# Performance work log

Hardware: AMD Instinct MI355X
Metric: run time of the kernel (lower is better)

## Reference

```python
import jax, jax.numpy as jnp
import numpy as np

B, H, W = 4, 1024, 1024

# 8-tap Sobel-style stencil: offsets in (u, v) units of (dx, dy)
OFF_U = jnp.array([-1.0, -1.0, -1.0, 0.0, 0.0, 1.0, 1.0, 1.0], dtype=jnp.float32)
OFF_V = jnp.array([-1.0, 0.0, 1.0, -1.0, 1.0, -1.0, 0.0, 1.0], dtype=jnp.float32)
KU = jnp.array([-0.25, -0.5, -0.25, 0.0, 0.0, 0.25, 0.5, 0.25], dtype=jnp.float32)
KV = jnp.array([-0.25, 0.0, 0.25, -0.5, 0.5, -0.25, 0.0, 0.25], dtype=jnp.float32)


def setup_inputs() -> dict:
    key = jax.random.key(0)
    k1, k2 = jax.random.split(key)
    x = jax.random.uniform(k1, (B, 3, H, W), dtype=jnp.float32)
    sigma = jax.random.uniform(k2, (B,), dtype=jnp.float32) * 2.0 + 0.5  # pixels
    return {"x": x, "sigma": sigma}


def _bilinear(tex, u, v):
    # tex: [3, H, W]; u, v: [8, H, W] normalized UV in [0,1]
    Hh, Ww = tex.shape[1], tex.shape[2]
    px = u * Ww - 0.5
    py = v * Hh - 0.5
    x0 = jnp.floor(px)
    y0 = jnp.floor(py)
    fx = (px - x0)[None]  # [1,8,H,W]
    fy = (py - y0)[None]
    x0i = jnp.clip(x0.astype(jnp.int32), 0, Ww - 1)
    x1i = jnp.clip(x0i + 1, 0, Ww - 1)
    y0i = jnp.clip(y0.astype(jnp.int32), 0, Hh - 1)
    y1i = jnp.clip(y0i + 1, 0, Hh - 1)
    t00 = tex[:, y0i, x0i]  # [3,8,H,W]
    t01 = tex[:, y0i, x1i]
    t10 = tex[:, y1i, x0i]
    t11 = tex[:, y1i, x1i]
    return (t00 * (1 - fx) * (1 - fy) + t01 * fx * (1 - fy)
            + t10 * (1 - fx) * fy + t11 * fx * fy)


def reference(x, sigma):
    Bb, C, Hh, Ww = x.shape
    ys, xs = jnp.meshgrid(jnp.arange(Hh, dtype=x.dtype),
                          jnp.arange(Ww, dtype=x.dtype), indexing='ij')
    u0 = (xs + 0.5) / Ww  # pixel-center UV
    v0 = (ys + 0.5) / Hh
    dx = sigma / Ww  # [B]
    dy = sigma / Hh
    u = u0[None, None] + OFF_U[None, :, None, None] * dx[:, None, None, None]  # [B,8,H,W]
    v = v0[None, None] + OFF_V[None, :, None, None] * dy[:, None, None, None]
    s = jax.vmap(_bilinear)(x, u, v)  # [B,3,8,H,W]
    s_u = jnp.einsum('bcthw,t->bchw', s, KU)
    s_v = jnp.einsum('bcthw,t->bchw', s, KV)
    lum = jnp.array([100.0, 1.0, 1.0], dtype=x.dtype)[None, :, None, None]
    s_u = s_u * lum
    s_v = s_v * lum
    # structure tensor components E, G, F
    return jnp.stack([(s_u * s_u).sum(1), (s_v * s_v).sum(1), (s_u * s_v).sum(1)], axis=1)
```

## Files before the change

kernel.cpp:

```cpp
#include <hip/hip_runtime.h>


#define W_ 1024
#define H_ 1024
#define PLANE (1 << 20)
#define TCOLS 64
#define TROWS 32
#define ROWS 8
#define LSTRIDE 72
#define NTILES 4
#define BUFSZ 9232

#define BX_ROWS 128
#define BX_SLOTS 134
#define BX_CH 1072
#define BX_NG 804

__device__ __forceinline__ float lerp1(float a, float b, float f) {
    return fmaf(f, b - a, a);
}

__device__ __forceinline__ void async_copy16(const float* g, float* s) {
    __builtin_amdgcn_global_load_lds(
        (const __attribute__((address_space(1))) unsigned int*)g,
        (__attribute__((address_space(3))) unsigned int*)s,
        16, 0, 0);
}

__device__ void slow_pixel(const float* __restrict__ Xb, float* __restrict__ Ob,
                           float sg, int xi, int y)
{
    float imf = floorf(-sg), ipf = floorf(sg);
    float fm  = -sg - imf;
    float fp  =  sg - ipf;
    int   im  = (int)imf, ip = (int)ipf;

    int cm0 = min(max(xi + im, 0), W_ - 1), cm1 = min(cm0 + 1, W_ - 1);
    int cp0 = min(max(xi + ip, 0), W_ - 1), cp1 = min(cp0 + 1, W_ - 1);
    int rm0 = min(max(y + im, 0), H_ - 1),  rm1 = min(rm0 + 1, H_ - 1);
    int rp0 = min(max(y + ip, 0), H_ - 1),  rp1 = min(rp0 + 1, H_ - 1);

    int o_rm0 = rm0 << 10, o_rm1 = rm1 << 10;
    int o_rp0 = rp0 << 10, o_rp1 = rp1 << 10;
    int o_r0  = y   << 10;

    float oxx = 0.f, oyy = 0.f, oxy = 0.f;

    #pragma unroll
    for (int c = 0; c < 3; ++c) {
        const float* base = Xb + ((size_t)c << 20);

        float hm_m0 = lerp1(base[o_rm0 + cm0], base[o_rm0 + cm1], fm);
        float hm_m1 = lerp1(base[o_rm1 + cm0], base[o_rm1 + cm1], fm);
        float hm_0  = lerp1(base[o_r0  + cm0], base[o_r0  + cm1], fm);
        float hm_p0 = lerp1(base[o_rp0 + cm0], base[o_rp0 + cm1], fm);
        float hm_p1 = lerp1(base[o_rp1 + cm0], base[o_rp1 + cm1], fm);
        float hp_m0 = lerp1(base[o_rm0 + cp0], base[o_rm0 + cp1], fp);
        float hp_m1 = lerp1(base[o_rm1 + cp0], base[o_rm1 + cp1], fp);
        float hp_0  = lerp1(base[o_r0  + cp0], base[o_r0  + cp1], fp);
        float hp_p0 = lerp1(base[o_rp0 + cp0], base[o_rp0 + cp1], fp);
        float hp_p1 = lerp1(base[o_rp1 + cp0], base[o_rp1 + cp1], fp);
        float h0_m0 = base[o_rm0 + xi], h0_m1 = base[o_rm1 + xi];
        float h0_p0 = base[o_rp0 + xi], h0_p1 = base[o_rp1 + xi];

        float t0 = lerp1(hm_m0, hm_m1, fm);
        float t1 = hm_0;
        float t2 = lerp1(hm_p0, hm_p1, fp);
        float t3 = lerp1(h0_m0, h0_m1, fm);
        float t4 = lerp1(h0_p0, h0_p1, fp);
        float t5 = lerp1(hp_m0, hp_m1, fm);
        float t6 = hp_0;
        float t7 = lerp1(hp_p0, hp_p1, fp);

        float su = 0.25f * (t5 + t7 - t0 - t2) + 0.5f * (t6 - t1);
        float sv = 0.25f * (t2 + t7 - t0 - t5) + 0.5f * (t4 - t3);

        float l2 = (c == 0) ? 10000.f : 1.f;
        oxx = fmaf(l2 * su, su, oxx);
        oyy = fmaf(l2 * sv, sv, oyy);
        oxy = fmaf(l2 * su, sv, oxy);
    }

    int pix = (y << 10) | xi;
    Ob[pix]             = oxx;
    Ob[PLANE + pix]     = oyy;
    Ob[2 * PLANE + pix] = oxy;
}

template<int IP>
__device__ void border_x_tile(const float* __restrict__ Xb, float* __restrict__ Ob,
                              float fp, float fm, int side, int y0b,
                              int tid, float* smem)
{
    const int cb = side ? (W_ - 8) : 0;
    constexpr int im = -IP - 1, ip = IP;

    #pragma unroll
    for (int it = 0; it < 3; ++it) {
        int g   = it * 256 + tid;
        int ch  = g / 268;
        int rem = g - ch * 268;
        int slot = rem >> 1, grp = rem & 1;
        int rr  = min(max(y0b - 3 + slot, 0), H_ - 1);
        async_copy16(Xb + ((size_t)ch << 20) + (rr << 10) + cb + grp * 4,
                     smem + g * 4);
    }
    {
        int g = 768 + tid;
        if (g < BX_NG) {
            int ch  = g / 268;
            int rem = g - ch * 268;
            int slot = rem >> 1, grp = rem & 1;
            int rr  = min(max(y0b - 3 + slot, 0), H_ - 1);
            async_copy16(Xb + ((size_t)ch << 20) + (rr << 10) + cb + grp * 4,
                         smem + g * 4);
        }
    }
    __syncthreads();

    #pragma unroll
    for (int it = 0; it < 2; ++it) {
        int p = it * 256 + tid;
        if (p < 3 * BX_ROWS) {
            int r   = p / 3;
            int cc_ = p - r * 3;
            int y   = y0b + r;
            int xi  = cb + (side ? 5 + cc_ : cc_);

            int cm0 = min(max(xi + im, 0), W_ - 1), cm1 = min(cm0 + 1, W_ - 1);
            int cp0 = min(max(xi + ip, 0), W_ - 1), cp1 = min(cp0 + 1, W_ - 1);
            int rm0 = min(max(y + im, 0), H_ - 1),  rm1 = min(rm0 + 1, H_ - 1);
            int rp0 = min(max(y + ip, 0), H_ - 1),  rp1 = min(rp0 + 1, H_ - 1);

            int s_m0 = (rm0 - y0b + 3) << 3, s_m1 = (rm1 - y0b + 3) << 3;
            int s_p0 = (rp0 - y0b + 3) << 3, s_p1 = (rp1 - y0b + 3) << 3;
            int s_0  = (y   - y0b + 3) << 3;
            int lm0 = cm0 - cb, lm1 = cm1 - cb;
            int lp0 = cp0 - cb, lp1 = cp1 - cb;
            int lxi = xi - cb;

            float oxx = 0.f, oyy = 0.f, oxy = 0.f;
            #pragma unroll
            for (int c = 0; c < 3; ++c) {
                const float* base = smem + c * BX_CH;

                float hm_m0 = lerp1(base[s_m0 + lm0], base[s_m0 + lm1], fm);
                float hm_m1 = lerp1(base[s_m1 + lm0], base[s_m1 + lm1], fm);
                float hm_0  = lerp1(base[s_0  + lm0], base[s_0  + lm1], fm);
                float hm_p0 = lerp1(base[s_p0 + lm0], base[s_p0 + lm1], fm);
                float hm_p1 = lerp1(base[s_p1 + lm0], base[s_p1 + lm1], fm);
                float hp_m0 = lerp1(base[s_m0 + lp0], base[s_m0 + lp1], fp);
                float hp_m1 = lerp1(base[s_m1 + lp0], base[s_m1 + lp1], fp);
                float hp_0  = lerp1(base[s_0  + lp0], base[s_0  + lp1], fp);
                float hp_p0 = lerp1(base[s_p0 + lp0], base[s_p0 + lp1], fp);
                float hp_p1 = lerp1(base[s_p1 + lp0], base[s_p1 + lp1], fp);
                float h0_m0 = base[s_m0 + lxi], h0_m1 = base[s_m1 + lxi];
                float h0_p0 = base[s_p0 + lxi], h0_p1 = base[s_p1 + lxi];

                float t0 = lerp1(hm_m0, hm_m1, fm);
                float t1 = hm_0;
                float t2 = lerp1(hm_p0, hm_p1, fp);
                float t3 = lerp1(h0_m0, h0_m1, fm);
                float t4 = lerp1(h0_p0, h0_p1, fp);
                float t5 = lerp1(hp_m0, hp_m1, fm);
                float t6 = hp_0;
                float t7 = lerp1(hp_p0, hp_p1, fp);

                float su = 0.25f * (t5 + t7 - t0 - t2) + 0.5f * (t6 - t1);
                float sv = 0.25f * (t2 + t7 - t0 - t5) + 0.5f * (t4 - t3);

                float l2 = (c == 0) ? 10000.f : 1.f;
                oxx = fmaf(l2 * su, su, oxx);
                oyy = fmaf(l2 * sv, sv, oyy);
                oxy = fmaf(l2 * su, sv, oxy);
            }

            int pix = (y << 10) | xi;
            Ob[pix]             = oxx;
            Ob[PLANE + pix]     = oyy;
            Ob[2 * PLANE + pix] = oxy;
        }
    }
}

template<int N>
__device__ __forceinline__ void acc(float (&arr)[N], int k, float val) {
    if (k >= 0 && k < N) arr[k] += val;
}

template<int IP>
__device__ void fast_tiles(const float* __restrict__ Xb, float* __restrict__ Ob,
                           float fp, float fm, int x0, int band0,
                           int tx, int ty, int tid, float* smem)
{
    constexpr int LROWS = TROWS + 2 * IP + 2;
    constexpr int RW    = ROWS + 2 * IP + 2;
    constexpr int NG    = 3 * LROWS * 18;
    constexpr int ITERS = (NG + 255) / 256;

    int x = x0 + tx;

    auto stage = [&](float* buf, int y0) {
        #pragma unroll
        for (int it = 0; it < ITERS; ++it) {
            int g    = min(it * 256 + tid, NG - 1);
            int row  = g / 18;
            int grp  = g - row * 18;
            int c    = row / LROWS;
            int lrow = row - c * LROWS;
            int gr   = min(max(y0 - IP - 1 + lrow, 0), H_ - 1);
            int gc   = min(max(x0 - 4 + grp * 4, 0), W_ - 4);
            async_copy16(Xb + ((size_t)c << 20) + (gr << 10) + gc,
                         buf + g * 4);
        }
    };

    stage(smem,         (band0 + 0) * TROWS);
    stage(smem + BUFSZ, (band0 + 1) * TROWS);

    #pragma unroll
    for (int t = 0; t < NTILES; ++t) {
        float* buf = smem + (t & 1) * BUFSZ;
        int y0 = (band0 + t) * TROWS;

        if constexpr (ITERS >= 9) asm volatile("s_waitcnt vmcnt(9)" ::: "memory");
        else                      asm volatile("s_waitcnt vmcnt(8)" ::: "memory");
        __builtin_amdgcn_s_barrier();

        float oxx[ROWS], oyy[ROWS], oxy[ROWS];
        #pragma unroll
        for (int k = 0; k < ROWS; ++k) { oxx[k] = 0.f; oyy[k] = 0.f; oxy[k] = 0.f; }

        const float* spb = buf + (ty * ROWS) * LSTRIDE + tx + (3 - IP);

        #pragma unroll
        for (int c = 0; c < 3; ++c) {
            const float* sp = spb + c * (LROWS * LSTRIDE);

            float vv[RW][5];
            #pragma unroll
            for (int w = 0; w < RW; ++w) {
                vv[w][0] = sp[w * LSTRIDE];
                vv[w][1] = sp[w * LSTRIDE + 1];
                vv[w][2] = sp[w * LSTRIDE + IP + 1];
                vv[w][3] = sp[w * LSTRIDE + 2 * IP + 1];
                vv[w][4] = sp[w * LSTRIDE + 2 * IP + 2];
            }

            float su[ROWS], sv[ROWS];
            #pragma unroll
            for (int k = 0; k < ROWS; ++k) { su[k] = 0.f; sv[k] = 0.f; }

            #pragma unroll
            for (int w = 0; w < RW; ++w) {
                float a0 = vv[w][0];
                float a1 = vv[w][1];
                float cc = vv[w][2];
                float b0 = vv[w][3];
                float b1 = vv[w][4];
                float hm = lerp1(a0, a1, fm);
                float hp = lerp1(b0, b1, fp);
                float q  = hp - hm;
                float A  = 0.25f * q;
                float hq = 0.5f  * q;
                float Bv = fmaf(0.25f, hm + hp, 0.5f * cc);
                float fpA = fp * A,  fmA = fm * A;
                float fpB = fp * Bv, fmB = fm * Bv;

                acc(su, w,              fpA);
                acc(su, w - 1,          fmA);
                acc(su, w - IP - 1,     hq);
                acc(su, w - 2*IP - 1,   fmA);
                acc(su, w - 2*IP - 2,   fpA);
                acc(sv, w,             -fpB);
                acc(sv, w - 1,         -fmB);
                acc(sv, w - 2*IP - 1,   fmB);
                acc(sv, w - 2*IP - 2,   fpB);
            }

            float l2 = (c == 0) ? 10000.f : 1.f;
            #pragma unroll
            for (int k = 0; k < ROWS; ++k) {
                oxx[k] = fmaf(l2 * su[k], su[k], oxx[k]);
                oyy[k] = fmaf(l2 * sv[k], sv[k], oyy[k]);
                oxy[k] = fmaf(l2 * su[k], sv[k], oxy[k]);
            }
        }

        bool okx = (x > IP) && (x < W_ - 1 - IP);
        int Y = y0 + ty * ROWS;
        #pragma unroll
        for (int k = 0; k < ROWS; ++k) {
            int y = Y + k;
            if (okx && y > IP) {
                int pix = (y << 10) | x;
                Ob[pix]             = oxx[k];
                Ob[PLANE + pix]     = oyy[k];
                Ob[2 * PLANE + pix] = oxy[k];
            }
        }

        asm volatile("s_waitcnt lgkmcnt(0)" ::: "memory");
        __builtin_amdgcn_s_barrier();
        if (t + 2 < NTILES)
            stage(buf, (band0 + t + 2) * TROWS);
    }
}

__global__ __launch_bounds__(256, 1) void st_kernel(
    const float* __restrict__ X, const float* __restrict__ S,
    float* __restrict__ O)
{
    int b  = blockIdx.z;
    const float* Xb = X + (size_t)b * 3 * PLANE;
    float*       Ob = O + (size_t)b * 3 * PLANE;
    float sg = S[b];

    int tx = threadIdx.x, ty = threadIdx.y;
    int tid = ty * 64 + tx;

    int ipv = (int)floorf(sg);
    int imv = (int)floorf(-sg);
    bool sig_ok = (imv == -ipv - 1) && ipv >= 0 && ipv <= 2;
    float fp = sg - (float)ipv;
    float fm = 1.0f - fp;

    __shared__ __align__(16) float smem[2 * BUFSZ];

    if (blockIdx.y == 0) {
        int side = blockIdx.x & 1;
        int y0b  = (blockIdx.x >> 1) * BX_ROWS;
        if (sig_ok) {
            switch (ipv) {
                case 0:  border_x_tile<0>(Xb, Ob, fp, fm, side, y0b, tid, smem); break;
                case 1:  border_x_tile<1>(Xb, Ob, fp, fm, side, y0b, tid, smem); break;
                default: border_x_tile<2>(Xb, Ob, fp, fm, side, y0b, tid, smem); break;
            }
        } else {
            for (int it = 0; it < 2; ++it) {
                int p = it * 256 + tid;
                if (p < 3 * BX_ROWS) {
                    int r = p / 3, cc = p - r * 3;
                    int xi = side ? 1021 + cc : cc;
                    slow_pixel(Xb, Ob, sg, xi, y0b + r);
                }
            }
        }
        return;
    }

    if (blockIdx.y == 1) {
        int p = blockIdx.x * 256 + tid;
        if (p < 3072) slow_pixel(Xb, Ob, sg, p & 1023, p >> 10);
        return;
    }

    int x0    = blockIdx.x * TCOLS;
    int band0 = (blockIdx.y - 2) * NTILES;

    if (sig_ok) {
        switch (ipv) {
            case 0:  fast_tiles<0>(Xb, Ob, fp, fm, x0, band0, tx, ty, tid, smem); break;
            case 1:  fast_tiles<1>(Xb, Ob, fp, fm, x0, band0, tx, ty, tid, smem); break;
            default: fast_tiles<2>(Xb, Ob, fp, fm, x0, band0, tx, ty, tid, smem); break;
        }
    } else {
        for (int t = 0; t < NTILES; ++t)
            for (int k = 0; k < ROWS; ++k)
                slow_pixel(Xb, Ob, sg, x0 + tx,
                           (band0 + t) * TROWS + ty * ROWS + k);
    }
}

extern "C" void kernel_launch(void* const* d_in, const int* in_sizes, int n_in,
                              void* d_out, int out_size, void* d_ws, size_t ws_size,
                              hipStream_t stream) {
    const float* x     = (const float*)d_in[0];
    const float* sigma = (const float*)d_in[1];
    float* out = (float*)d_out;

    dim3 grid(W_ / TCOLS, H_ / TROWS / NTILES + 2, 4), block(64, 4);
    hipLaunchKernelGGL(st_kernel, grid, block, 0, stream, x, sigma, out);
}
```

Before: 109.1 us.

## Remap threads to 4-column by 2-row micro-tiles with float4 LDS reads

Each thread now computes a 4-wide by 2-row output micro-tile instead of a 1-wide by 8-row column strip. Each stencil row is read from LDS as three float4 loads that serve four output columns, and the LDS row stride and staging groups change to fit the wider halo. The aim is fewer LDS load instructions and better horizontal reuse. The trade-off is more vertical halo rows recomputed per thread (RW grows relative to KR) and stores that are no longer one contiguous column per lane, which may reduce write coalescing.

```diff
diff --git a/kernel.cpp b/kernel.cpp
--- a/kernel.cpp
+++ b/kernel.cpp
@@ -7,9 +7,11 @@
 #define TCOLS 64
 #define TROWS 32
 #define ROWS 8
-#define LSTRIDE 72
+#define KR 2
+#define LSTRIDE 76
+#define GPR 19
 #define NTILES 4
-#define BUFSZ 9232
+#define BUFSZ 9216
 
 #define BX_ROWS 128
 #define BX_SLOTS 134
@@ -184,8 +186,8 @@
 }
 
 template<int N>
-__device__ __forceinline__ void acc(float (&arr)[N], int k, float val) {
-    if (k >= 0 && k < N) arr[k] += val;
+__device__ __forceinline__ void accf(float (&arr)[N], int k, float w, float v) {
+    if (k >= 0 && k < N) arr[k] = fmaf(w, v, arr[k]);
 }
 
 template<int IP>
@@ -194,18 +196,22 @@
                            int tx, int ty, int tid, float* smem)
 {
     constexpr int LROWS = TROWS + 2 * IP + 2;
-    constexpr int RW    = ROWS + 2 * IP + 2;
-    constexpr int NG    = 3 * LROWS * 18;
+    constexpr int RW    = KR + 2 * IP + 2;
+    constexpr int NG    = 3 * LROWS * GPR;
     constexpr int ITERS = (NG + 255) / 256;
 
-    int x = x0 + tx;
+    const int xg = tx & 15;
+    const int yg = ty * 4 + (tx >> 4);
+    const int X  = xg << 2;
+    const int gx = x0 + X;
+    const float fp4 = 0.25f * fp, fm4 = 0.25f * fm;
 
     auto stage = [&](float* buf, int y0) {
         #pragma unroll
         for (int it = 0; it < ITERS; ++it) {
             int g    = min(it * 256 + tid, NG - 1);
-            int row  = g / 18;
-            int grp  = g - row * 18;
+            int row  = g / GPR;
+            int grp  = g - row * GPR;
             int c    = row / LROWS;
             int lrow = row - c * LROWS;
             int gr   = min(max(y0 - IP - 1 + lrow, 0), H_ - 1);
@@ -227,76 +233,80 @@
         else                      asm volatile("s_waitcnt vmcnt(8)" ::: "memory");
         __builtin_amdgcn_s_barrier();
 
-        float oxx[ROWS], oyy[ROWS], oxy[ROWS];
-        #pragma unroll
-        for (int k = 0; k < ROWS; ++k) { oxx[k] = 0.f; oyy[k] = 0.f; oxy[k] = 0.f; }
-
-        const float* spb = buf + (ty * ROWS) * LSTRIDE + tx + (3 - IP);
+        float oxx[4][KR], oyy[4][KR], oxy[4][KR];
+        #pragma unroll
+        for (int c4 = 0; c4 < 4; ++c4)
+            #pragma unroll
+            for (int k = 0; k < KR; ++k)
+                { oxx[c4][k] = 0.f; oyy[c4][k] = 0.f; oxy[c4][k] = 0.f; }
 
         #pragma unroll
         for (int c = 0; c < 3; ++c) {
-            const float* sp = spb + c * (LROWS * LSTRIDE);
-
-            float vv[RW][5];
+            const float* sp = buf + (c * LROWS + yg * KR) * LSTRIDE + X;
+
+            float su[4][KR], sv[4][KR];
+            #pragma unroll
+            for (int c4 = 0; c4 < 4; ++c4)
+                #pragma unroll
+                for (int k = 0; k < KR; ++k) { su[c4][k] = 0.f; sv[c4][k] = 0.f; }
+
             #pragma unroll
             for (int w = 0; w < RW; ++w) {
-                vv[w][0] = sp[w * LSTRIDE];
-                vv[w][1] = sp[w * LSTRIDE + 1];
-                vv[w][2] = sp[w * LSTRIDE + IP + 1];
-                vv[w][3] = sp[w * LSTRIDE + 2 * IP + 1];
-                vv[w][4] = sp[w * LSTRIDE + 2 * IP + 2];
-            }
-
-            float su[ROWS], sv[ROWS];
-            #pragma unroll
-            for (int k = 0; k < ROWS; ++k) { su[k] = 0.f; sv[k] = 0.f; }
-
-            #pragma unroll
-            for (int w = 0; w < RW; ++w) {
-                float a0 = vv[w][0];
-                float a1 = vv[w][1];
-                float cc = vv[w][2];
-                float b0 = vv[w][3];
-                float b1 = vv[w][4];
-                float hm = lerp1(a0, a1, fm);
-                float hp = lerp1(b0, b1, fp);
-                float q  = hp - hm;
-                float A  = 0.25f * q;
-                float hq = 0.5f  * q;
-                float Bv = fmaf(0.25f, hm + hp, 0.5f * cc);
-                float fpA = fp * A,  fmA = fm * A;
-                float fpB = fp * Bv, fmB = fm * Bv;
-
-                acc(su, w,              fpA);
-                acc(su, w - 1,          fmA);
-                acc(su, w - IP - 1,     hq);
-                acc(su, w - 2*IP - 1,   fmA);
-                acc(su, w - 2*IP - 2,   fpA);
-                acc(sv, w,             -fpB);
-                acc(sv, w - 1,         -fmB);
-                acc(sv, w - 2*IP - 1,   fmB);
-                acc(sv, w - 2*IP - 2,   fpB);
+                const float4 q0 = *reinterpret_cast<const float4*>(sp + w * LSTRIDE);
+                const float4 q1 = *reinterpret_cast<const float4*>(sp + w * LSTRIDE + 4);
+                const float4 q2 = *reinterpret_cast<const float4*>(sp + w * LSTRIDE + 8);
+                float v[12] = {q0.x, q0.y, q0.z, q0.w,
+                               q1.x, q1.y, q1.z, q1.w,
+                               q2.x, q2.y, q2.z, q2.w};
+                #pragma unroll
+                for (int c4 = 0; c4 < 4; ++c4) {
+                    float a0 = v[c4 + 3 - IP], a1 = v[c4 + 4 - IP];
+                    float cc = v[c4 + 4];
+                    float b0 = v[c4 + 4 + IP], b1 = v[c4 + 5 + IP];
+                    float hm = lerp1(a0, a1, fm);
+                    float hp = lerp1(b0, b1, fp);
+                    float d  = hp - hm;
+                    float e  = fmaf(0.5f, cc, 0.25f * (hm + hp));
+                    accf(su[c4], w,              fp4,  d);
+                    accf(su[c4], w - 1,          fm4,  d);
+                    accf(su[c4], w - IP - 1,     0.5f, d);
+                    accf(su[c4], w - 2*IP - 1,   fm4,  d);
+                    accf(su[c4], w - 2*IP - 2,   fp4,  d);
+                    accf(sv[c4], w,             -fp,   e);
+                    accf(sv[c4], w - 1,         -fm,   e);
+                    accf(sv[c4], w - 2*IP - 1,   fm,   e);
+                    accf(sv[c4], w - 2*IP - 2,   fp,   e);
+                }
             }
 
             float l2 = (c == 0) ? 10000.f : 1.f;
             #pragma unroll
-            for (int k = 0; k < ROWS; ++k) {
-                oxx[k] = fmaf(l2 * su[k], su[k], oxx[k]);
-                oyy[k] = fmaf(l2 * sv[k], sv[k], oyy[k]);
-                oxy[k] = fmaf(l2 * su[k], sv[k], oxy[k]);
-            }
-        }
-
-        bool okx = (x > IP) && (x < W_ - 1 - IP);
-        int Y = y0 + ty * ROWS;
-        #pragma unroll
-        for (int k = 0; k < ROWS; ++k) {
-            int y = Y + k;
-            if (okx && y > IP) {
-                int pix = (y << 10) | x;
-                Ob[pix]             = oxx[k];
-                Ob[PLANE + pix]     = oyy[k];
-                Ob[2 * PLANE + pix] = oxy[k];
+            for (int c4 = 0; c4 < 4; ++c4)
+                #pragma unroll
+                for (int k = 0; k < KR; ++k) {
+                    oxx[c4][k] = fmaf(l2 * su[c4][k], su[c4][k], oxx[c4][k]);
+                    oyy[c4][k] = fmaf(l2 * sv[c4][k], sv[c4][k], oyy[c4][k]);
+                    oxy[c4][k] = fmaf(l2 * su[c4][k], sv[c4][k], oxy[c4][k]);
+                }
+        }
+
+        bool okc[4];
+        #pragma unroll
+        for (int c4 = 0; c4 < 4; ++c4)
+            okc[c4] = (gx + c4 > IP) && (gx + c4 < W_ - 1 - IP);
+        #pragma unroll
+        for (int k = 0; k < KR; ++k) {
+            int y = y0 + yg * KR + k;
+            if (y > IP) {
+                int pix = (y << 10) + gx;
+                #pragma unroll
+                for (int c4 = 0; c4 < 4; ++c4) {
+                    if (okc[c4]) {
+                        Ob[pix + c4]             = oxx[c4][k];
+                        Ob[PLANE + pix + c4]     = oyy[c4][k];
+                        Ob[2 * PLANE + pix + c4] = oxy[c4][k];
+                    }
+                }
             }
         }
 
```

After: 123.4 us. 13.1% more time.

## Replace persistent double-buffered tile loop with one tile per block at higher occupancy

Applied to the files above, without the earlier changes.

Removes the 4-tile persistent loop with double-buffered async LDS staging. Each block now loads a single tile, synchronizes and computes, and the grid grows fourfold. Launch bounds go from 1 to 4 blocks per CU, and the shared buffer is sized for one tile, so latency is hidden by running more waves instead of by software pipelining. The cost is more block launches, halo reloads and per-block setup, and loads no longer overlap compute within a block.

```diff
diff --git a/kernel.cpp b/kernel.cpp
--- a/kernel.cpp
+++ b/kernel.cpp
@@ -8,8 +8,6 @@
 #define TROWS 32
 #define ROWS 8
 #define LSTRIDE 72
-#define NTILES 4
-#define BUFSZ 9232
 
 #define BX_ROWS 128
 #define BX_SLOTS 134
@@ -189,125 +187,101 @@
 }
 
 template<int IP>
-__device__ void fast_tiles(const float* __restrict__ Xb, float* __restrict__ Ob,
-                           float fp, float fm, int x0, int band0,
-                           int tx, int ty, int tid, float* smem)
+__device__ void fast_tile(const float* __restrict__ Xb, float* __restrict__ Ob,
+                          float fp, float fm, int x0, int y0,
+                          int tx, int ty, int tid, float* smem)
 {
-    constexpr int LROWS = TROWS + 2 * IP + 2;
-    constexpr int RW    = ROWS + 2 * IP + 2;
-    constexpr int NG    = 3 * LROWS * 18;
-    constexpr int ITERS = (NG + 255) / 256;
+    constexpr int LROWS  = TROWS + 2 * IP + 2;
+    constexpr int RW     = ROWS + 2 * IP + 2;
+    constexpr int NG     = 3 * LROWS * 18;
+    constexpr int FULLIT = NG / 256;
 
     int x = x0 + tx;
-
-    auto stage = [&](float* buf, int y0) {
+    int Y = y0 + ty * ROWS;
+
+    auto stage = [&](int g) {
+        int row  = g / 18;
+        int grp  = g - row * 18;
+        int c    = row / LROWS;
+        int lrow = row - c * LROWS;
+        int gr   = min(max(y0 - IP - 1 + lrow, 0), H_ - 1);
+        int gc   = min(max(x0 - 4 + grp * 4, 0), W_ - 4);
+        async_copy16(Xb + ((size_t)c << 20) + (gr << 10) + gc,
+                     smem + g * 4);
+    };
+
+    #pragma unroll
+    for (int it = 0; it < FULLIT; ++it)
+        stage(it * 256 + tid);
+    if (FULLIT * 256 + tid < NG)
+        stage(FULLIT * 256 + tid);
+
+    __syncthreads();
+
+    float oxx[ROWS], oyy[ROWS], oxy[ROWS];
+    #pragma unroll
+    for (int k = 0; k < ROWS; ++k) { oxx[k] = 0.f; oyy[k] = 0.f; oxy[k] = 0.f; }
+
+    const float* spb = smem + (ty * ROWS) * LSTRIDE + tx + (3 - IP);
+
+    #pragma unroll
+    for (int c = 0; c < 3; ++c) {
+        const float* sp = spb + c * (LROWS * LSTRIDE);
+
+        float su[ROWS], sv[ROWS];
         #pragma unroll
-        for (int it = 0; it < ITERS; ++it) {
-            int g    = min(it * 256 + tid, NG - 1);
-            int row  = g / 18;
-            int grp  = g - row * 18;
-            int c    = row / LROWS;
-            int lrow = row - c * LROWS;
-            int gr   = min(max(y0 - IP - 1 + lrow, 0), H_ - 1);
-            int gc   = min(max(x0 - 4 + grp * 4, 0), W_ - 4);
-            async_copy16(Xb + ((size_t)c << 20) + (gr << 10) + gc,
-                         buf + g * 4);
-        }
-    };
-
-    stage(smem,         (band0 + 0) * TROWS);
-    stage(smem + BUFSZ, (band0 + 1) * TROWS);
-
-    #pragma unroll
-    for (int t = 0; t < NTILES; ++t) {
-        float* buf = smem + (t & 1) * BUFSZ;
-        int y0 = (band0 + t) * TROWS;
-
-        if constexpr (ITERS >= 9) asm volatile("s_waitcnt vmcnt(9)" ::: "memory");
-        else                      asm volatile("s_waitcnt vmcnt(8)" ::: "memory");
-        __builtin_amdgcn_s_barrier();
-
-        float oxx[ROWS], oyy[ROWS], oxy[ROWS];
+        for (int k = 0; k < ROWS; ++k) { su[k] = 0.f; sv[k] = 0.f; }
+
         #pragma unroll
-        for (int k = 0; k < ROWS; ++k) { oxx[k] = 0.f; oyy[k] = 0.f; oxy[k] = 0.f; }
-
-        const float* spb = buf + (ty * ROWS) * LSTRIDE + tx + (3 - IP);
-
-        #pragma unroll
-        for (int c = 0; c < 3; ++c) {
-            const float* sp = spb + c * (LROWS * LSTRIDE);
-
-            float vv[RW][5];
-            #pragma unroll
-            for (int w = 0; w < RW; ++w) {
-                vv[w][0] = sp[w * LSTRIDE];
-                vv[w][1] = sp[w * LSTRIDE + 1];
-                vv[w][2] = sp[w * LSTRIDE + IP + 1];
-                vv[w][3] = sp[w * LSTRIDE + 2 * IP + 1];
-                vv[w][4] = sp[w * LSTRIDE + 2 * IP + 2];
-            }
-
-            float su[ROWS], sv[ROWS];
-            #pragma unroll
-            for (int k = 0; k < ROWS; ++k) { su[k] = 0.f; sv[k] = 0.f; }
-
-            #pragma unroll
-            for (int w = 0; w < RW; ++w) {
-                float a0 = vv[w][0];
-                float a1 = vv[w][1];
-                float cc = vv[w][2];
-                float b0 = vv[w][3];
-                float b1 = vv[w][4];
-                float hm = lerp1(a0, a1, fm);
-                float hp = lerp1(b0, b1, fp);
-                float q  = hp - hm;
-                float A  = 0.25f * q;
-                float hq = 0.5f  * q;
-                float Bv = fmaf(0.25f, hm + hp, 0.5f * cc);
-                float fpA = fp * A,  fmA = fm * A;
-                float fpB = fp * Bv, fmB = fm * Bv;
-
-                acc(su, w,              fpA);
-                acc(su, w - 1,          fmA);
-                acc(su, w - IP - 1,     hq);
-                acc(su, w - 2*IP - 1,   fmA);
-                acc(su, w - 2*IP - 2,   fpA);
-                acc(sv, w,             -fpB);
-                acc(sv, w - 1,         -fmB);
-                acc(sv, w - 2*IP - 1,   fmB);
-                acc(sv, w - 2*IP - 2,   fpB);
-            }
-
-            float l2 = (c == 0) ? 10000.f : 1.f;
-            #pragma unroll
-            for (int k = 0; k < ROWS; ++k) {
-                oxx[k] = fmaf(l2 * su[k], su[k], oxx[k]);
-                oyy[k] = fmaf(l2 * sv[k], sv[k], oyy[k]);
-                oxy[k] = fmaf(l2 * su[k], sv[k], oxy[k]);
-            }
-        }
-
-        bool okx = (x > IP) && (x < W_ - 1 - IP);
-        int Y = y0 + ty * ROWS;
+        for (int w = 0; w < RW; ++w) {
+            float a0 = sp[w * LSTRIDE];
+            float a1 = sp[w * LSTRIDE + 1];
+            float cc = sp[w * LSTRIDE + IP + 1];
+            float b0 = sp[w * LSTRIDE + 2 * IP + 1];
+            float b1 = sp[w * LSTRIDE + 2 * IP + 2];
+            float hm = lerp1(a0, a1, fm);
+            float hp = lerp1(b0, b1, fp);
+            float q  = hp - hm;
+            float A  = 0.25f * q;
+            float hq = 0.5f  * q;
+            float Bv = fmaf(0.25f, hm + hp, 0.5f * cc);
+            float fpA = fp * A,  fmA = fm * A;
+            float fpB = fp * Bv, fmB = fm * Bv;
+
+            acc(su, w,              fpA);
+            acc(su, w - 1,          fmA);
+            acc(su, w - IP - 1,     hq);
+            acc(su, w - 2*IP - 1,   fmA);
+            acc(su, w - 2*IP - 2,   fpA);
+            acc(sv, w,             -fpB);
+            acc(sv, w - 1,         -fmB);
+            acc(sv, w - 2*IP - 1,   fmB);
+            acc(sv, w - 2*IP - 2,   fpB);
+        }
+
+        float l2 = (c == 0) ? 10000.f : 1.f;
         #pragma unroll
         for (int k = 0; k < ROWS; ++k) {
-            int y = Y + k;
-            if (okx && y > IP) {
-                int pix = (y << 10) | x;
-                Ob[pix]             = oxx[k];
-                Ob[PLANE + pix]     = oyy[k];
-                Ob[2 * PLANE + pix] = oxy[k];
-            }
-        }
-
-        asm volatile("s_waitcnt lgkmcnt(0)" ::: "memory");
-        __builtin_amdgcn_s_barrier();
-        if (t + 2 < NTILES)
-            stage(buf, (band0 + t + 2) * TROWS);
-    }
-}
-
-__global__ __launch_bounds__(256, 1) void st_kernel(
+            oxx[k] = fmaf(l2 * su[k], su[k], oxx[k]);
+            oyy[k] = fmaf(l2 * sv[k], sv[k], oyy[k]);
+            oxy[k] = fmaf(l2 * su[k], sv[k], oxy[k]);
+        }
+    }
+
+    bool okx = (x > IP) && (x < W_ - 1 - IP);
+    #pragma unroll
+    for (int k = 0; k < ROWS; ++k) {
+        int y = Y + k;
+        if (okx && y > IP) {
+            int pix = (y << 10) | x;
+            Ob[pix]             = oxx[k];
+            Ob[PLANE + pix]     = oyy[k];
+            Ob[2 * PLANE + pix] = oxy[k];
+        }
+    }
+}
+
+__global__ __launch_bounds__(256, 4) void st_kernel(
     const float* __restrict__ X, const float* __restrict__ S,
     float* __restrict__ O)
 {
@@ -325,7 +299,7 @@
     float fp = sg - (float)ipv;
     float fm = 1.0f - fp;
 
-    __shared__ __align__(16) float smem[2 * BUFSZ];
+    __shared__ __align__(16) float smem[3 * (TROWS + 6) * LSTRIDE];
 
     if (blockIdx.y == 0) {
         int side = blockIdx.x & 1;
@@ -355,20 +329,18 @@
         return;
     }
 
-    int x0    = blockIdx.x * TCOLS;
-    int band0 = (blockIdx.y - 2) * NTILES;
+    int x0 = blockIdx.x * TCOLS;
+    int y0 = (blockIdx.y - 2) * TROWS;
 
     if (sig_ok) {
         switch (ipv) {
-            case 0:  fast_tiles<0>(Xb, Ob, fp, fm, x0, band0, tx, ty, tid, smem); break;
-            case 1:  fast_tiles<1>(Xb, Ob, fp, fm, x0, band0, tx, ty, tid, smem); break;
-            default: fast_tiles<2>(Xb, Ob, fp, fm, x0, band0, tx, ty, tid, smem); break;
+            case 0:  fast_tile<0>(Xb, Ob, fp, fm, x0, y0, tx, ty, tid, smem); break;
+            case 1:  fast_tile<1>(Xb, Ob, fp, fm, x0, y0, tx, ty, tid, smem); break;
+            default: fast_tile<2>(Xb, Ob, fp, fm, x0, y0, tx, ty, tid, smem); break;
         }
     } else {
-        for (int t = 0; t < NTILES; ++t)
-            for (int k = 0; k < ROWS; ++k)
-                slow_pixel(Xb, Ob, sg, x0 + tx,
-                           (band0 + t) * TROWS + ty * ROWS + k);
+        for (int k = 0; k < ROWS; ++k)
+            slow_pixel(Xb, Ob, sg, x0 + tx, y0 + ty * ROWS + k);
     }
 }
 
@@ -379,6 +351,6 @@
     const float* sigma = (const float*)d_in[1];
     float* out = (float*)d_out;
 
-    dim3 grid(W_ / TCOLS, H_ / TROWS / NTILES + 2, 4), block(64, 4);
+    dim3 grid(W_ / TCOLS, H_ / TROWS + 2, 4), block(64, 4);
     hipLaunchKernelGGL(st_kernel, grid, block, 0, stream, x, sigma, out);
 }
```

Measured after the change: 130.6 us. 19.8% more time.
